# Kernel tuning notes

Measured on AMD Instinct MI355X. Metric: run time of the kernel, lower is better.

Reference implementation:

```python
import jax, jax.numpy as jnp
import numpy as np

INPUT_DIM = 1024
OUTPUT_DIM = 1024
DEGREE = 8
N_TOKENS = 8192


def setup_inputs() -> dict:
    key = jax.random.key(0)
    k1, k2 = jax.random.split(key)
    x = jax.random.normal(k1, (N_TOKENS, INPUT_DIM), dtype=jnp.float32)
    # xavier_normal_ with gain = 1/(input_dim*(degree+1)) over fan dims (output_dim, degree+1)
    fan_in, fan_out = OUTPUT_DIM, DEGREE + 1  # torch treats dim0/dim1 as fans; scale is tiny anyway
    gain = 1.0 / (INPUT_DIM * (DEGREE + 1))
    std = gain * np.sqrt(2.0 / (INPUT_DIM + OUTPUT_DIM))
    cheby_coeffs = std * jax.random.normal(k2, (INPUT_DIM, OUTPUT_DIM, DEGREE + 1), dtype=jnp.float32)
    return {"x": x, "cheby_coeffs": cheby_coeffs}


def reference(x, cheby_coeffs):
    # x: (..., input_dim) -> y: (..., output_dim)
    degree_p1 = cheby_coeffs.shape[-1]
    theta = jnp.arccos(jnp.tanh(x))                      # (..., i)
    arange = jnp.arange(degree_p1, dtype=x.dtype)        # (d,)
    basis = jnp.cos(theta[..., None] * arange)           # (..., i, d) Chebyshev T_d(tanh(x))
    y = jnp.einsum('...id,iod->...o', basis, cheby_coeffs)
    return y
```

## Files before the change

kernel.cpp:

```cpp
#include <hip/hip_runtime.h>


typedef __bf16 bf16;
typedef __bf16 bf16x8 __attribute__((ext_vector_type(8)));
typedef float f32x2 __attribute__((ext_vector_type(2)));
typedef float f32x4 __attribute__((ext_vector_type(4)));
typedef float f32x16 __attribute__((ext_vector_type(16)));

#define MFMA __builtin_amdgcn_mfma_f32_32x32x16_bf16

__device__ __forceinline__ void g2lds16(const void* g, void* l) {
  __builtin_amdgcn_global_load_lds(
      (const __attribute__((address_space(1))) unsigned int*)g,
      (__attribute__((address_space(3))) unsigned int*)l, 16, 0, 0);
}

__device__ __forceinline__ float fast_tanh(float a) {
  float e = __expf(a + a);
  return 1.f - 2.f * __builtin_amdgcn_rcpf(e + 1.f);
}


__global__ __launch_bounds__(256)
void cheby_prep2(const float* __restrict__ x, const float* __restrict__ C,
                 bf16* __restrict__ A, bf16* __restrict__ B,
                 float* __restrict__ bias_p) {
  const int bid = blockIdx.x, tid = threadIdx.x;
  if (bid < 512) {
    const int mb = bid >> 3, ig = bid & 7;
    const int rl = tid & 127, ih = tid >> 7;
    const int m32 = rl >> 5, ml = rl & 31;
    const int i_base = ig * 128 + ih * 64;
    const float* xp = x + (size_t)(mb * 128 + rl) * 1024 + i_base;
    bf16* aout = A + (size_t)mb * 128 * 8192;
    #pragma unroll 2
    for (int q = 0; q < 16; ++q) {
      f32x4 xv = *(const f32x4*)(xp + q * 4);
      #pragma unroll
      for (int j = 0; j < 4; ++j) {
        const int ia = i_base + q * 4 + j;
        const int kt = ia >> 3, cc = ia & 7;
        float z = fast_tanh(xv[j]);
        float z2 = z + z, pv = 1.f, cv = z;
        bf16x8 v;
        #pragma unroll
        for (int d = 0; d < 8; ++d) {
          v[d] = (bf16)cv;
          float nx = z2 * cv - pv; pv = cv; cv = nx;
        }
        const int widx = (((cc >> 1) * 4 + m32) * 2 + (cc & 1)) * 32 + ml;
        *(bf16x8*)(aout + (size_t)kt * 8192 + widx * 8) = v;
      }
    }
    return;
  }
  const int b2 = bid - 512;
  __shared__ float tile[32][292];
  const int i0 = (b2 >> 5) * 32, o0 = (b2 & 31) * 32;
  {
    const int r = tid >> 3, seg = tid & 7;
    const float* src = C + (size_t)(i0 + r) * 9216 + (size_t)o0 * 9 + seg * 36;
    float* dst = &tile[r][seg * 36];
    #pragma unroll
    for (int v = 0; v < 9; ++v) *(f32x4*)(dst + v * 4) = *(const f32x4*)(src + v * 4);
  }
  __syncthreads();
  #pragma unroll
  for (int j = 0; j < 4; ++j) {
    int e = tid + 256 * j;
    int il = e >> 5, ol = e & 31;
    int i = i0 + il, o = o0 + ol;
    bf16x8 v;
    #pragma unroll
    for (int d = 0; d < 8; ++d) v[d] = (bf16)tile[il][ol * 9 + 1 + d];
    const int cc = i & 7;
    size_t tnum = (size_t)(o >> 7) * 128 + (i >> 3);
    const int widx = (((cc >> 1) * 4 + ((o & 127) >> 5)) * 2 + (cc & 1)) * 32 + (o & 31);
    *(bf16x8*)(B + tnum * 8192 + widx * 8) = v;
  }
  if (tid < 32) {
    float s = 0.f;
    #pragma unroll
    for (int i = 0; i < 32; ++i) s += tile[i][tid * 9];
    bias_p[(size_t)(b2 >> 5) * 1024 + o0 + tid] = s;
  }
}

__global__ __launch_bounds__(256, 2)
void cheby_gemm2(const bf16* __restrict__ A, const bf16* __restrict__ B,
                 const float* __restrict__ bias_p, float* __restrict__ out) {
  __shared__ bf16 As[2][8192];
  const int tid = threadIdx.x;
  const int lane = tid & 63, w = tid >> 6;
  const int wm = w >> 1, wn = w & 1;
  const int bid = blockIdx.x;
  const int mb = (bid & 7) * 8 + ((bid >> 3) & 7);
  const int nb = bid >> 6;

  const bf16* aG = A + (size_t)mb * 128 * 8192 + (w * 4) * 512 + lane * 8;
  const bf16* bG = B + (size_t)nb * 128 * 8192 + wn * 1024 + lane * 8;

  f32x16 acc[2][2];
  #pragma unroll
  for (int a = 0; a < 2; ++a)
    #pragma unroll
    for (int b = 0; b < 2; ++b)
      #pragma unroll
      for (int r = 0; r < 16; ++r) acc[a][b][r] = 0.f;

  bf16x8 bA[4][2], bB[4][2];

  auto issueA = [&](int t, int p) {
    const bf16* g = aG + (size_t)t * 8192;
    #pragma unroll
    for (int c = 0; c < 4; ++c)
      g2lds16(g + c * 512, &As[p][(w * 4 + c) * 512]);
  };
  auto loadB = [&](bf16x8 (&dst)[4][2], int t) {
    const bf16* g = bG + (size_t)t * 8192;
    #pragma unroll
    for (int ks = 0; ks < 4; ++ks)
      #pragma unroll
      for (int nt = 0; nt < 2; ++nt)
        dst[ks][nt] = *(const bf16x8*)(g + (ks * 256 + nt * 64) * 8);
  };

  issueA(0, 0);
  loadB(bA, 0);
  loadB(bB, 1);

  auto tilestep = [&](int t, int p, bf16x8 (&cur)[4][2]) {
    const bf16* aL = &As[p][(wm * 128 + lane) * 8];
    if (t + 1 < 128) {
      issueA(t + 1, p ^ 1);
      asm volatile("s_waitcnt vmcnt(12)" ::: "memory");
    } else {
      asm volatile("s_waitcnt vmcnt(0)" ::: "memory");
    }
    __builtin_amdgcn_s_barrier();
    asm volatile("" ::: "memory");
    {
      bf16x8 a00 = *(const bf16x8*)(aL);
      bf16x8 a01 = *(const bf16x8*)(aL + 64 * 8);
      bf16x8 a10 = *(const bf16x8*)(aL + 256 * 8);
      bf16x8 a11 = *(const bf16x8*)(aL + 320 * 8);
      __builtin_amdgcn_s_setprio(1);
      acc[0][0] = MFMA(a00, cur[0][0], acc[0][0], 0, 0, 0);
      acc[0][1] = MFMA(a00, cur[0][1], acc[0][1], 0, 0, 0);
      acc[1][0] = MFMA(a01, cur[0][0], acc[1][0], 0, 0, 0);
      acc[1][1] = MFMA(a01, cur[0][1], acc[1][1], 0, 0, 0);
      acc[0][0] = MFMA(a10, cur[1][0], acc[0][0], 0, 0, 0);
      acc[0][1] = MFMA(a10, cur[1][1], acc[0][1], 0, 0, 0);
      acc[1][0] = MFMA(a11, cur[1][0], acc[1][0], 0, 0, 0);
      acc[1][1] = MFMA(a11, cur[1][1], acc[1][1], 0, 0, 0);
      __builtin_amdgcn_s_setprio(0);
    }
    asm volatile("" ::: "memory");
    __builtin_amdgcn_s_barrier();
    asm volatile("" ::: "memory");
    {
      bf16x8 a20 = *(const bf16x8*)(aL + 512 * 8);
      bf16x8 a21 = *(const bf16x8*)(aL + 576 * 8);
      bf16x8 a30 = *(const bf16x8*)(aL + 768 * 8);
      bf16x8 a31 = *(const bf16x8*)(aL + 832 * 8);
      __builtin_amdgcn_s_setprio(1);
      acc[0][0] = MFMA(a20, cur[2][0], acc[0][0], 0, 0, 0);
      acc[0][1] = MFMA(a20, cur[2][1], acc[0][1], 0, 0, 0);
      acc[1][0] = MFMA(a21, cur[2][0], acc[1][0], 0, 0, 0);
      acc[1][1] = MFMA(a21, cur[2][1], acc[1][1], 0, 0, 0);
      acc[0][0] = MFMA(a30, cur[3][0], acc[0][0], 0, 0, 0);
      acc[0][1] = MFMA(a30, cur[3][1], acc[0][1], 0, 0, 0);
      acc[1][0] = MFMA(a31, cur[3][0], acc[1][0], 0, 0, 0);
      acc[1][1] = MFMA(a31, cur[3][1], acc[1][1], 0, 0, 0);
      __builtin_amdgcn_s_setprio(0);
    }
    if (t + 2 < 128) loadB(cur, t + 2);
    asm volatile("" ::: "memory");
    __builtin_amdgcn_s_barrier();
    asm volatile("" ::: "memory");
  };

  #pragma unroll 1
  for (int t2 = 0; t2 < 128; t2 += 2) {
    tilestep(t2, 0, bA);
    tilestep(t2 + 1, 1, bB);
  }

  const int h = lane >> 5, ml = lane & 31;
  const int c0 = nb * 128 + wn * 64 + ml;
  float bv0 = 0.f, bv1 = 0.f;
  #pragma unroll
  for (int p = 0; p < 32; ++p) {
    bv0 += bias_p[(size_t)p * 1024 + c0];
    bv1 += bias_p[(size_t)p * 1024 + c0 + 32];
  }
  #pragma unroll
  for (int mt = 0; mt < 2; ++mt)
    #pragma unroll
    for (int r = 0; r < 16; ++r) {
      int row = mb * 128 + wm * 64 + mt * 32 + (r & 3) + 8 * (r >> 2) + 4 * h;
      float* po = out + (size_t)row * 1024 + c0;
      po[0]  = acc[mt][0][r] + bv0;
      po[32] = acc[mt][1][r] + bv1;
    }
}

__global__ __launch_bounds__(256)
void cheby_prep(const float* __restrict__ x, const float* __restrict__ C,
                bf16* __restrict__ Bt, float* __restrict__ bias_p,
                float* __restrict__ th) {
  const int bid = blockIdx.x, tid = threadIdx.x;
  if (bid >= 1024) {
    const int r = bid - 1024;
    f32x4 v = *(const f32x4*)(x + (size_t)r * 1024 + tid * 4);
    f32x4 t;
    #pragma unroll
    for (int j = 0; j < 4; ++j) t[j] = fast_tanh(v[j]);
    *(f32x2*)(th + (size_t)r * 1024 + tid * 2)       = (f32x2){t.x, t.z};
    *(f32x2*)(th + (size_t)r * 1024 + 512 + tid * 2) = (f32x2){t.y, t.w};
    return;
  }
  __shared__ float tile[32][292];
  const int i0 = (bid >> 5) * 32, o0 = (bid & 31) * 32;
  {
    const int r = tid >> 3, seg = tid & 7;
    const float* src = C + (size_t)(i0 + r) * 9216 + (size_t)o0 * 9 + seg * 36;
    float* dst = &tile[r][seg * 36];
    #pragma unroll
    for (int v = 0; v < 9; ++v) *(f32x4*)(dst + v * 4) = *(const f32x4*)(src + v * 4);
  }
  __syncthreads();
  #pragma unroll
  for (int j = 0; j < 4; ++j) {
    int e = tid + 256 * j;
    int il = e >> 5, ol = e & 31;
    int i = i0 + il, o = o0 + ol;
    bf16x8 v;
    #pragma unroll
    for (int d = 0; d < 8; ++d) v[d] = (bf16)tile[il][ol * 9 + 1 + d];
    size_t idx16 = ((size_t)((o >> 7) * 128 + (i >> 3)) * 8 + (i & 7)) * 128 + (o & 127);
    *(bf16x8*)&Bt[idx16 * 8] = v;
  }
  if (tid < 32) {
    float s = 0.f;
    #pragma unroll
    for (int i = 0; i < 32; ++i) s += tile[i][tid * 9];
    bias_p[(size_t)(bid >> 5) * 1024 + o0 + tid] = s;
  }
}

__global__ __launch_bounds__(256, 2)
void cheby_gemm(const float* __restrict__ th, const bf16* __restrict__ Bt,
                const float* __restrict__ bias_p, float* __restrict__ out) {
  __shared__ bf16 Bs[2][8192];
  const int tid  = threadIdx.x;
  const int lane = tid & 63, w = tid >> 6;
  const int wm = w >> 1, wn = w & 1;
  const int nb = blockIdx.x & 7, mb = blockIdx.x >> 3;
  const int t0 = mb * 128, o0 = nb * 128;
  const int ml = lane & 31, h = lane >> 5;

  const float* xr0 = th + (size_t)(t0 + wm * 64 + ml) * 1024 + h * 512;
  const float* xr1 = xr0 + 32 * 1024;
  const bf16* btw = Bt + ((size_t)nb * 128 * 1024 + (size_t)w * 256 + lane) * 8;

  f32x16 acc[2][2];
  #pragma unroll
  for (int a = 0; a < 2; ++a)
    #pragma unroll
    for (int b = 0; b < 2; ++b)
      #pragma unroll
      for (int r = 0; r < 16; ++r) acc[a][b][r] = 0.f;

  bf16x8 afrA[2][4], afrB[2][4];
  f32x4 xv0, xv1;

  auto gen = [&](bf16x8 (&dst)[2][4], f32x4 s0, f32x4 s1) {
    #pragma unroll
    for (int ks = 0; ks < 4; ++ks) {
      f32x2 t  = {s0[ks], s1[ks]};
      f32x2 t2 = t + t;
      f32x2 prev = {1.f, 1.f}, cur = t;
      #pragma unroll
      for (int j = 0; j < 8; ++j) {
        dst[0][ks][j] = (bf16)cur.x;
        dst[1][ks][j] = (bf16)cur.y;
        f32x2 nx = t2 * cur - prev;
        prev = cur; cur = nx;
      }
    }
  };

  {
    f32x4 s0 = *(const f32x4*)(xr0), s1 = *(const f32x4*)(xr1);
    gen(afrA, s0, s1);
    xv0 = *(const f32x4*)(xr0 + 4);
    xv1 = *(const f32x4*)(xr1 + 4);
  }
  #pragma unroll
  for (int b = 0; b < 4; ++b)
    g2lds16(btw + (size_t)b * 64 * 8, &Bs[0][(w * 256 + b * 64) * 8]);

  auto stage = [&](int s, int bi, bf16x8 (&cur)[2][4], bf16x8 (&nxt)[2][4]) {
    __syncthreads();
    if (s < 127) {
      const bf16* g = btw + (size_t)(s + 1) * 8192;
      #pragma unroll
      for (int b = 0; b < 4; ++b)
        g2lds16(g + (size_t)b * 64 * 8, &Bs[bi ^ 1][(w * 256 + b * 64) * 8]);
    }
    bf16x8 bfr[4][2];
    #pragma unroll
    for (int ks = 0; ks < 4; ++ks) {
      const int ce = ((ks * 2 + h) * 128 + wn * 64 + ml) * 8;
      bfr[ks][0] = *(const bf16x8*)&Bs[bi][ce];
      bfr[ks][1] = *(const bf16x8*)&Bs[bi][ce + 32 * 8];
    }
    if (s < 127) {
      gen(nxt, xv0, xv1);
      if (s < 126) {
        xv0 = *(const f32x4*)(xr0 + (s + 2) * 4);
        xv1 = *(const f32x4*)(xr1 + (s + 2) * 4);
      }
    }
    #pragma unroll
    for (int ks = 0; ks < 4; ++ks) {
      acc[0][0] = MFMA(cur[0][ks], bfr[ks][0], acc[0][0], 0, 0, 0);
      acc[0][1] = MFMA(cur[0][ks], bfr[ks][1], acc[0][1], 0, 0, 0);
      acc[1][0] = MFMA(cur[1][ks], bfr[ks][0], acc[1][0], 0, 0, 0);
      acc[1][1] = MFMA(cur[1][ks], bfr[ks][1], acc[1][1], 0, 0, 0);
    }
  };

  #pragma unroll 1
  for (int s2 = 0; s2 < 64; ++s2) {
    stage(2 * s2,     0, afrA, afrB);
    stage(2 * s2 + 1, 1, afrB, afrA);
  }

  const int c0 = o0 + wn * 64 + ml;
  float bv0 = 0.f, bv1 = 0.f;
  #pragma unroll
  for (int p = 0; p < 32; ++p) {
    bv0 += bias_p[(size_t)p * 1024 + c0];
    bv1 += bias_p[(size_t)p * 1024 + c0 + 32];
  }
  #pragma unroll
  for (int mt = 0; mt < 2; ++mt)
    #pragma unroll
    for (int r = 0; r < 16; ++r) {
      int row = t0 + wm * 64 + mt * 32 + (r & 3) + 8 * (r >> 2) + 4 * h;
      float* po = out + (size_t)row * 1024 + c0;
      po[0]  = acc[mt][0][r] + bv0;
      po[32] = acc[mt][1][r] + bv1;
    }
}

__global__ __launch_bounds__(256)
void cheby_naive(const float* __restrict__ x, const float* __restrict__ C,
                 float* __restrict__ out) {
  const int t = blockIdx.x, tid = threadIdx.x;
  float acc[4] = {0.f, 0.f, 0.f, 0.f};
  for (int i = 0; i < 1024; ++i) {
    float th = tanhf(x[(size_t)t * 1024 + i]);
    float T[9]; T[0] = 1.f; T[1] = th;
    #pragma unroll
    for (int d = 2; d < 9; ++d) T[d] = 2.f * th * T[d - 1] - T[d - 2];
    #pragma unroll
    for (int j = 0; j < 4; ++j) {
      const float* cp = &C[((size_t)i * 1024 + tid + j * 256) * 9];
      float s = 0.f;
      #pragma unroll
      for (int d = 0; d < 9; ++d) s += T[d] * cp[d];
      acc[j] += s;
    }
  }
  #pragma unroll
  for (int j = 0; j < 4; ++j) out[(size_t)t * 1024 + tid + j * 256] = acc[j];
}

extern "C" void kernel_launch(void* const* d_in, const int* in_sizes, int n_in,
                              void* d_out, int out_size, void* d_ws, size_t ws_size,
                              hipStream_t stream) {
  (void)in_sizes; (void)n_in; (void)out_size;
  const float* x = (const float*)d_in[0];
  const float* C = (const float*)d_in[1];
  float* out = (float*)d_out;

  const size_t a_bytes  = (size_t)8192 * 8192 * 2;
  const size_t b_bytes  = (size_t)8 * 128 * 8192 * 2;
  const size_t bp_bytes = (size_t)32 * 1024 * 4;

  const size_t bt_bytes = (size_t)8 * 128 * 1024 * 8 * 2;
  const size_t th_bytes = (size_t)8192 * 1024 * 4;

  if (ws_size >= a_bytes + b_bytes + bp_bytes) {
    bf16*  A      = (bf16*)d_ws;
    bf16*  B      = (bf16*)((char*)d_ws + a_bytes);
    float* bias_p = (float*)((char*)d_ws + a_bytes + b_bytes);
    cheby_prep2<<<1536, 256, 0, stream>>>(x, C, A, B, bias_p);
    cheby_gemm2<<<512, 256, 0, stream>>>(A, B, bias_p, out);
  } else if (ws_size >= bt_bytes + bp_bytes + th_bytes) {
    bf16*  Bt     = (bf16*)d_ws;
    float* bias_p = (float*)((char*)d_ws + bt_bytes);
    float* th     = (float*)((char*)d_ws + bt_bytes + bp_bytes);
    cheby_prep<<<9216, 256, 0, stream>>>(x, C, Bt, bias_p, th);
    cheby_gemm<<<512, 256, 0, stream>>>(th, Bt, bias_p, out);
  } else {
    cheby_naive<<<8192, 256, 0, stream>>>(x, C, out);
  }
}
```

Measured before the change: 286.4 us.

## Enlarge GEMM tile to 256 rows with 512 threads and quad-buffered A prefetch

The GEMM kernel now uses 512-thread workgroups covering 256 rows by 128 columns. A tiles are staged through four LDS buffers with a prefetch distance of two tiles, and the barrier and waitcnt schedule is reworked around that. The prep kernel splits its feature-expansion work across twice as many blocks. The goals are more reuse of each B tile per workgroup and more latency hiding for global-to-LDS loads, at the cost of 128KB of LDS per block, which may limit occupancy, and a more fragile wait schedule.

Measured after the change: 289.3 us. About the same (+1.0%).

```diff
diff --git a/kernel.cpp b/kernel.cpp
--- a/kernel.cpp
+++ b/kernel.cpp
@@ -20,21 +20,20 @@
   return 1.f - 2.f * __builtin_amdgcn_rcpf(e + 1.f);
 }
 
-
 __global__ __launch_bounds__(256)
 void cheby_prep2(const float* __restrict__ x, const float* __restrict__ C,
                  bf16* __restrict__ A, bf16* __restrict__ B,
                  float* __restrict__ bias_p) {
   const int bid = blockIdx.x, tid = threadIdx.x;
-  if (bid < 512) {
-    const int mb = bid >> 3, ig = bid & 7;
+  if (bid < 1024) {
+    const int mb = bid >> 4, ig = bid & 15;
     const int rl = tid & 127, ih = tid >> 7;
     const int m32 = rl >> 5, ml = rl & 31;
-    const int i_base = ig * 128 + ih * 64;
+    const int i_base = ig * 64 + ih * 32;
     const float* xp = x + (size_t)(mb * 128 + rl) * 1024 + i_base;
     bf16* aout = A + (size_t)mb * 128 * 8192;
     #pragma unroll 2
-    for (int q = 0; q < 16; ++q) {
+    for (int q = 0; q < 8; ++q) {
       f32x4 xv = *(const f32x4*)(xp + q * 4);
       #pragma unroll
       for (int j = 0; j < 4; ++j) {
@@ -54,7 +53,7 @@
     }
     return;
   }
-  const int b2 = bid - 512;
+  const int b2 = bid - 1024;
   __shared__ float tile[32][292];
   const int i0 = (b2 >> 5) * 32, o0 = (b2 & 31) * 32;
   {
@@ -86,18 +85,23 @@
   }
 }
 
-__global__ __launch_bounds__(256, 2)
-void cheby_gemm2(const bf16* __restrict__ A, const bf16* __restrict__ B,
+__global__ __launch_bounds__(512, 2)
+void cheby_gemm3(const bf16* __restrict__ A, const bf16* __restrict__ B,
                  const float* __restrict__ bias_p, float* __restrict__ out) {
-  __shared__ bf16 As[2][8192];
+  __shared__ bf16 As[4][16384];
   const int tid = threadIdx.x;
   const int lane = tid & 63, w = tid >> 6;
   const int wm = w >> 1, wn = w & 1;
   const int bid = blockIdx.x;
-  const int mb = (bid & 7) * 8 + ((bid >> 3) & 7);
-  const int nb = bid >> 6;
-
-  const bf16* aG = A + (size_t)mb * 128 * 8192 + (w * 4) * 512 + lane * 8;
+  const int wgid = (bid & 7) * 32 + (bid >> 3);
+  const int mb2 = wgid >> 3, nb = wgid & 7;
+
+  const int ml = lane & 31, h = lane >> 5;
+  const int aoff = h * 256 + ml * 8;
+  const int sBase0 = ((wm * 64) >> 7) * 8192 + ((wm * 2) & 3) * 512;
+  const int sBase1 = (((wm * 64 + 32) >> 7)) * 8192 + ((wm * 2 + 1) & 3) * 512;
+
+  const bf16* aG = A + (size_t)(mb2 * 2) * 128 * 8192 + tid * 8;
   const bf16* bG = B + (size_t)nb * 128 * 8192 + wn * 1024 + lane * 8;
 
   f32x16 acc[2][2];
@@ -110,11 +114,13 @@
 
   bf16x8 bA[4][2], bB[4][2];
 
-  auto issueA = [&](int t, int p) {
-    const bf16* g = aG + (size_t)t * 8192;
-    #pragma unroll
-    for (int c = 0; c < 4; ++c)
-      g2lds16(g + c * 512, &As[p][(w * 4 + c) * 512]);
+  auto issueA2 = [&](int t, int buf, int cp) {
+    #pragma unroll
+    for (int cc2 = 0; cc2 < 2; ++cc2) {
+      const int c = cp * 2 + cc2;
+      g2lds16(aG + (size_t)(c >> 1) * 1048576 + (size_t)t * 8192 + (c & 1) * 4096,
+              &As[buf][c * 4096 + tid * 8]);
+    }
   };
   auto loadB = [&](bf16x8 (&dst)[4][2], int t) {
     const bf16* g = bG + (size_t)t * 8192;
@@ -125,68 +131,67 @@
         dst[ks][nt] = *(const bf16x8*)(g + (ks * 256 + nt * 64) * 8);
   };
 
-  issueA(0, 0);
-  loadB(bA, 0);
-  loadB(bB, 1);
-
-  auto tilestep = [&](int t, int p, bf16x8 (&cur)[4][2]) {
-    const bf16* aL = &As[p][(wm * 128 + lane) * 8];
-    if (t + 1 < 128) {
-      issueA(t + 1, p ^ 1);
-      asm volatile("s_waitcnt vmcnt(12)" ::: "memory");
-    } else {
-      asm volatile("s_waitcnt vmcnt(0)" ::: "memory");
-    }
-    __builtin_amdgcn_s_barrier();
-    asm volatile("" ::: "memory");
+  issueA2(0, 0, 0); issueA2(0, 0, 1);
+  issueA2(1, 1, 0); issueA2(1, 1, 1);
+  loadB(bA, 0); loadB(bB, 1);
+  asm volatile("s_waitcnt vmcnt(20)" ::: "memory");
+  __builtin_amdgcn_s_barrier();
+
+  auto step = [&](int t, int buf, bf16x8 (&bfr)[4][2]) {
+    const bf16* asb = &As[buf][0];
     {
-      bf16x8 a00 = *(const bf16x8*)(aL);
-      bf16x8 a01 = *(const bf16x8*)(aL + 64 * 8);
-      bf16x8 a10 = *(const bf16x8*)(aL + 256 * 8);
-      bf16x8 a11 = *(const bf16x8*)(aL + 320 * 8);
+      bf16x8 a00 = *(const bf16x8*)(asb + sBase0 + 0 * 2048 + aoff);
+      bf16x8 a10 = *(const bf16x8*)(asb + sBase1 + 0 * 2048 + aoff);
+      bf16x8 a01 = *(const bf16x8*)(asb + sBase0 + 1 * 2048 + aoff);
+      bf16x8 a11 = *(const bf16x8*)(asb + sBase1 + 1 * 2048 + aoff);
+      if (t < 126) issueA2(t + 2, (t + 2) & 3, 0);
+      __builtin_amdgcn_s_barrier();
       __builtin_amdgcn_s_setprio(1);
-      acc[0][0] = MFMA(a00, cur[0][0], acc[0][0], 0, 0, 0);
-      acc[0][1] = MFMA(a00, cur[0][1], acc[0][1], 0, 0, 0);
-      acc[1][0] = MFMA(a01, cur[0][0], acc[1][0], 0, 0, 0);
-      acc[1][1] = MFMA(a01, cur[0][1], acc[1][1], 0, 0, 0);
-      acc[0][0] = MFMA(a10, cur[1][0], acc[0][0], 0, 0, 0);
-      acc[0][1] = MFMA(a10, cur[1][1], acc[0][1], 0, 0, 0);
-      acc[1][0] = MFMA(a11, cur[1][0], acc[1][0], 0, 0, 0);
-      acc[1][1] = MFMA(a11, cur[1][1], acc[1][1], 0, 0, 0);
+      acc[0][0] = MFMA(a00, bfr[0][0], acc[0][0], 0, 0, 0);
+      acc[0][1] = MFMA(a00, bfr[0][1], acc[0][1], 0, 0, 0);
+      acc[1][0] = MFMA(a10, bfr[0][0], acc[1][0], 0, 0, 0);
+      acc[1][1] = MFMA(a10, bfr[0][1], acc[1][1], 0, 0, 0);
+      acc[0][0] = MFMA(a01, bfr[1][0], acc[0][0], 0, 0, 0);
+      acc[0][1] = MFMA(a01, bfr[1][1], acc[0][1], 0, 0, 0);
+      acc[1][0] = MFMA(a11, bfr[1][0], acc[1][0], 0, 0, 0);
+      acc[1][1] = MFMA(a11, bfr[1][1], acc[1][1], 0, 0, 0);
       __builtin_amdgcn_s_setprio(0);
-    }
-    asm volatile("" ::: "memory");
-    __builtin_amdgcn_s_barrier();
-    asm volatile("" ::: "memory");
+      __builtin_amdgcn_s_barrier();
+    }
     {
-      bf16x8 a20 = *(const bf16x8*)(aL + 512 * 8);
-      bf16x8 a21 = *(const bf16x8*)(aL + 576 * 8);
-      bf16x8 a30 = *(const bf16x8*)(aL + 768 * 8);
-      bf16x8 a31 = *(const bf16x8*)(aL + 832 * 8);
+      bf16x8 a02 = *(const bf16x8*)(asb + sBase0 + 2 * 2048 + aoff);
+      bf16x8 a12 = *(const bf16x8*)(asb + sBase1 + 2 * 2048 + aoff);
+      bf16x8 a03 = *(const bf16x8*)(asb + sBase0 + 3 * 2048 + aoff);
+      bf16x8 a13 = *(const bf16x8*)(asb + sBase1 + 3 * 2048 + aoff);
+      if (t < 126) issueA2(t + 2, (t + 2) & 3, 1);
+      if (t < 126)       asm volatile("s_waitcnt vmcnt(12)" ::: "memory");
+      else if (t == 126) asm volatile("s_waitcnt vmcnt(8)" ::: "memory");
+      else               asm volatile("s_waitcnt vmcnt(0)" ::: "memory");
+      __builtin_amdgcn_s_barrier();
       __builtin_amdgcn_s_setprio(1);
-      acc[0][0] = MFMA(a20, cur[2][0], acc[0][0], 0, 0, 0);
-      acc[0][1] = MFMA(a20, cur[2][1], acc[0][1], 0, 0, 0);
-      acc[1][0] = MFMA(a21, cur[2][0], acc[1][0], 0, 0, 0);
-      acc[1][1] = MFMA(a21, cur[2][1], acc[1][1], 0, 0, 0);
-      acc[0][0] = MFMA(a30, cur[3][0], acc[0][0], 0, 0, 0);
-      acc[0][1] = MFMA(a30, cur[3][1], acc[0][1], 0, 0, 0);
-      acc[1][0] = MFMA(a31, cur[3][0], acc[1][0], 0, 0, 0);
-      acc[1][1] = MFMA(a31, cur[3][1], acc[1][1], 0, 0, 0);
+      acc[0][0] = MFMA(a02, bfr[2][0], acc[0][0], 0, 0, 0);
+      acc[0][1] = MFMA(a02, bfr[2][1], acc[0][1], 0, 0, 0);
+      acc[1][0] = MFMA(a12, bfr[2][0], acc[1][0], 0, 0, 0);
+      acc[1][1] = MFMA(a12, bfr[2][1], acc[1][1], 0, 0, 0);
+      acc[0][0] = MFMA(a03, bfr[3][0], acc[0][0], 0, 0, 0);
+      acc[0][1] = MFMA(a03, bfr[3][1], acc[0][1], 0, 0, 0);
+      acc[1][0] = MFMA(a13, bfr[3][0], acc[1][0], 0, 0, 0);
+      acc[1][1] = MFMA(a13, bfr[3][1], acc[1][1], 0, 0, 0);
       __builtin_amdgcn_s_setprio(0);
-    }
-    if (t + 2 < 128) loadB(cur, t + 2);
-    asm volatile("" ::: "memory");
-    __builtin_amdgcn_s_barrier();
-    asm volatile("" ::: "memory");
+      if (t < 126) loadB(bfr, t + 2);
+      __builtin_amdgcn_s_barrier();
+    }
   };
 
   #pragma unroll 1
-  for (int t2 = 0; t2 < 128; t2 += 2) {
-    tilestep(t2, 0, bA);
-    tilestep(t2 + 1, 1, bB);
-  }
-
-  const int h = lane >> 5, ml = lane & 31;
+  for (int it = 0; it < 32; ++it) {
+    const int t = it * 4;
+    step(t,     0, bA);
+    step(t + 1, 1, bB);
+    step(t + 2, 2, bA);
+    step(t + 3, 3, bB);
+  }
+
   const int c0 = nb * 128 + wn * 64 + ml;
   float bv0 = 0.f, bv1 = 0.f;
   #pragma unroll
@@ -194,11 +199,12 @@
     bv0 += bias_p[(size_t)p * 1024 + c0];
     bv1 += bias_p[(size_t)p * 1024 + c0 + 32];
   }
+  const int r0 = mb2 * 256 + wm * 64;
   #pragma unroll
   for (int mt = 0; mt < 2; ++mt)
     #pragma unroll
     for (int r = 0; r < 16; ++r) {
-      int row = mb * 128 + wm * 64 + mt * 32 + (r & 3) + 8 * (r >> 2) + 4 * h;
+      int row = r0 + mt * 32 + (r & 3) + 8 * (r >> 2) + 4 * h;
       float* po = out + (size_t)row * 1024 + c0;
       po[0]  = acc[mt][0][r] + bv0;
       po[32] = acc[mt][1][r] + bv1;
@@ -398,8 +404,8 @@
     bf16*  A      = (bf16*)d_ws;
     bf16*  B      = (bf16*)((char*)d_ws + a_bytes);
     float* bias_p = (float*)((char*)d_ws + a_bytes + b_bytes);
-    cheby_prep2<<<1536, 256, 0, stream>>>(x, C, A, B, bias_p);
-    cheby_gemm2<<<512, 256, 0, stream>>>(A, B, bias_p, out);
+    cheby_prep2<<<2048, 256, 0, stream>>>(x, C, A, B, bias_p);
+    cheby_gemm3<<<256, 512, 0, stream>>>(A, B, bias_p, out);
   } else if (ws_size >= bt_bytes + bp_bytes + th_bytes) {
     bf16*  Bt     = (bf16*)d_ws;
     float* bias_p = (float*)((char*)d_ws + bt_bytes);
```
